# Kernel optimization log

Hardware: AMD Instinct MI355X
Metric: run time of the kernel (lower is better)

The kernel has to match this reference:

```python
import jax, jax.numpy as jnp
import numpy as np

B, L, SH, EH, A, T = 128, 200, 512, 512, 512, 3


def setup_inputs() -> dict:
    key = jax.random.key(0)
    ks = jax.random.split(key, 13)
    s = 0.05  # small init scale to keep tanh/sigmoid unsaturated
    return {
        "sent_enc_doc": jax.random.normal(ks[0], (B, L, 2 * SH), jnp.float32),
        "h0_w": jax.random.normal(ks[1], (EH, SH), jnp.float32) * s,
        "h0_b": jax.random.normal(ks[2], (EH,), jnp.float32) * s,
        "gru_w_ih": jax.random.normal(ks[3], (3 * EH, 2 * SH), jnp.float32) * s,
        "gru_w_hh": jax.random.normal(ks[4], (3 * EH, EH), jnp.float32) * s,
        "gru_b_ih": jax.random.normal(ks[5], (3 * EH,), jnp.float32) * s,
        "gru_b_hh": jax.random.normal(ks[6], (3 * EH,), jnp.float32) * s,
        "wq": jax.random.normal(ks[7], (A, EH), jnp.float32) * s,
        "bq": jax.random.normal(ks[8], (A,), jnp.float32) * s,
        "wd": jax.random.normal(ks[9], (A, 2 * SH), jnp.float32) * s,
        "bd": jax.random.normal(ks[10], (A,), jnp.float32) * s,
        "ws": jax.random.normal(ks[11], (1, A), jnp.float32) * s,
        "bs": jax.random.normal(ks[12], (1,), jnp.float32) * s,
    }


def reference(sent_enc_doc, h0_w, h0_b, gru_w_ih, gru_w_hh, gru_b_ih, gru_b_hh,
              wq, bq, wd, bd, ws, bs):
    b, l, d2 = sent_enc_doc.shape
    sh = d2 // 2
    eh = gru_w_hh.shape[1]
    neg = jnp.asarray(-1e6, sent_enc_doc.dtype)

    # h0 = tanh(W * last backward vector), replicated across doc_len
    last_back = sent_enc_doc[:, 0, sh:]                      # (B, SH)
    h0 = jnp.tanh(last_back @ h0_w.T + h0_b)                 # (B, EH)
    h = jnp.broadcast_to(h0[:, None, :], (b, l, eh))         # (B, L, EH)

    s_prev = jnp.zeros((b, l, d2), sent_enc_doc.dtype)
    d_proj = sent_enc_doc @ wd.T + bd                        # (B, L, A) - loop-invariant
    mask = jnp.zeros((b, l), bool)
    rows = jnp.arange(b)

    scores_list, sel_list = [], []
    for _ in range(T):  # fixed, tiny, sequentially-dependent loop
        # GRUCell (torch gate order: r, z, n)
        gx = s_prev @ gru_w_ih.T + gru_b_ih                  # (B, L, 3EH)
        gh = h @ gru_w_hh.T + gru_b_hh                       # (B, L, 3EH)
        xr, xz, xn = jnp.split(gx, 3, axis=-1)
        hr, hz, hn = jnp.split(gh, 3, axis=-1)
        r = jax.nn.sigmoid(xr + hr)
        z = jax.nn.sigmoid(xz + hz)
        n = jnp.tanh(xn + r * hn)
        h = (1.0 - z) * n + z * h                            # (B, L, EH)

        # scorer: ws . tanh(Wq h + Wd s_i)
        score = (jnp.tanh(h @ wq.T + bq + d_proj) @ ws.T + bs)[..., 0]  # (B, L)
        score = jnp.where(mask, neg, score)
        idx = jnp.argmax(score, axis=1)                      # (B,)
        mask = mask.at[rows, idx].set(True)

        # gather the selected sentence encoding, broadcast to all positions
        s_sel = jnp.take_along_axis(sent_enc_doc, idx[:, None, None], axis=1)  # (B,1,2SH)
        s_prev = jnp.broadcast_to(s_sel, (b, l, d2))

        scores_list.append(score)
        sel_list.append(idx)

    sents_scores = jnp.stack(scores_list, axis=1)            # (B, T, L)
    sents_selected = jnp.stack(sel_list, axis=1)             # (B, T)
    return sents_scores, sents_selected
```

## Files before the change

kernel.cpp:

```cpp
#include <hip/hip_runtime.h>
#include <hip/hip_bf16.h>

constexpr int Bn  = 128;
constexpr int Ln  = 200;
constexpr int D2n = 1024;
constexpr int G3n = 1536;
constexpr int Tn  = 3;
constexpr int Nn  = 512;
constexpr int Kn  = 1024;

typedef unsigned short ushort;
typedef float f32x4 __attribute__((ext_vector_type(4)));
typedef __bf16 bf16x8 __attribute__((ext_vector_type(8)));

__device__ __forceinline__ ushort f2bf(float f) {
  unsigned u = __float_as_uint(f);
  unsigned r = (u + 0x7fffu + ((u >> 16) & 1u)) >> 16;
  return (ushort)r;
}
__device__ __forceinline__ float bf2f(ushort h) {
  return __uint_as_float(((unsigned)h) << 16);
}

__global__ void k_gather_lastb(const float* __restrict__ sent, float* __restrict__ lastb) {
  int i = blockIdx.x * 256 + threadIdx.x;
  int b = i >> 9, k = i & 511;
  lastb[i] = sent[(size_t)b * (Ln * D2n) + 512 + k];
}

__global__ void k_splitW(const float* __restrict__ W, ushort* __restrict__ hi,
                         ushort* __restrict__ lo) {
  int i = blockIdx.x * 256 + threadIdx.x;
  float4 v = ((const float4*)W)[i];
  ushort4 h, l;
  h.x = f2bf(v.x); l.x = f2bf(v.x - bf2f(h.x));
  h.y = f2bf(v.y); l.y = f2bf(v.y - bf2f(h.y));
  h.z = f2bf(v.z); l.z = f2bf(v.z - bf2f(h.z));
  h.w = f2bf(v.w); l.w = f2bf(v.w - bf2f(h.w));
  ((ushort4*)hi)[i] = h;
  ((ushort4*)lo)[i] = l;
}

template<int K, int ACT>
__launch_bounds__(256)
__global__ void k_small_gemm(const float* __restrict__ in, const float* __restrict__ W,
                             const float* __restrict__ bias, float* __restrict__ out, int J) {
  __shared__ float s[16 * K];
  const int b0 = blockIdx.y * 16;
  const int jl = threadIdx.x & 63;
  const int j  = blockIdx.x * 64 + jl;
  const int bg = (threadIdx.x >> 6) * 4;

  const float4* inp4 = (const float4*)(in + (size_t)b0 * K);
  float4* s4 = (float4*)s;
  for (int i = threadIdx.x; i < 4 * K; i += 256) s4[i] = inp4[i];
  __syncthreads();

  const float4* w4 = (const float4*)(W + (size_t)j * K);
  const float4* r0 = (const float4*)(s + (size_t)(bg + 0) * K);
  const float4* r1 = (const float4*)(s + (size_t)(bg + 1) * K);
  const float4* r2 = (const float4*)(s + (size_t)(bg + 2) * K);
  const float4* r3 = (const float4*)(s + (size_t)(bg + 3) * K);

  float acc0 = 0.f, acc1 = 0.f, acc2 = 0.f, acc3 = 0.f;
  #pragma unroll 4
  for (int k4 = 0; k4 < K / 4; ++k4) {
    float4 wv = w4[k4];
    float4 a;
    a = r0[k4]; acc0 += wv.x*a.x + wv.y*a.y + wv.z*a.z + wv.w*a.w;
    a = r1[k4]; acc1 += wv.x*a.x + wv.y*a.y + wv.z*a.z + wv.w*a.w;
    a = r2[k4]; acc2 += wv.x*a.x + wv.y*a.y + wv.z*a.z + wv.w*a.w;
    a = r3[k4]; acc3 += wv.x*a.x + wv.y*a.y + wv.z*a.z + wv.w*a.w;
  }
  float bb = bias[j];
  float v;
  v = acc0 + bb; if (ACT) v = tanhf(v); out[(size_t)(b0 + bg + 0) * J + j] = v;
  v = acc1 + bb; if (ACT) v = tanhf(v); out[(size_t)(b0 + bg + 1) * J + j] = v;
  v = acc2 + bb; if (ACT) v = tanhf(v); out[(size_t)(b0 + bg + 2) * J + j] = v;
  v = acc3 + bb; if (ACT) v = tanhf(v); out[(size_t)(b0 + bg + 3) * J + j] = v;
}

constexpr int LDW = 40;
__launch_bounds__(256)
__global__ void k_dproj_mfma(const float* __restrict__ A, const ushort* __restrict__ Whi,
                             const ushort* __restrict__ Wlo, const float* __restrict__ bias,
                             float* __restrict__ C) {
  __shared__ __align__(16) ushort Ah[128][LDW];
  __shared__ __align__(16) ushort Al[128][LDW];
  __shared__ __align__(16) ushort Bh[128][LDW];
  __shared__ __align__(16) ushort Bl[128][LDW];

  const int m0 = blockIdx.x * 128, n0 = blockIdx.y * 128;
  const int tid  = threadIdx.x;
  const int wave = tid >> 6, lane = tid & 63;
  const int wy = (wave >> 1) * 64, wx = (wave & 1) * 64;
  const int lm = lane & 15, lq = lane >> 4;

  const int sr   = tid >> 1;
  const int sk   = (tid & 1) * 16;

  f32x4 acc[4][4] = {};

  const float* Arow = A + (size_t)(m0 + sr) * Kn + sk;
  const ushort* Bhrow = Whi + (size_t)(n0 + sr) * Kn + sk;
  const ushort* Blrow = Wlo + (size_t)(n0 + sr) * Kn + sk;

  for (int k0 = 0; k0 < Kn; k0 += 32) {
    #pragma unroll
    for (int i = 0; i < 4; ++i) {
      float4 v = *(const float4*)(Arow + k0 + i * 4);
      ushort4 h, l;
      h.x = f2bf(v.x); l.x = f2bf(v.x - bf2f(h.x));
      h.y = f2bf(v.y); l.y = f2bf(v.y - bf2f(h.y));
      h.z = f2bf(v.z); l.z = f2bf(v.z - bf2f(h.z));
      h.w = f2bf(v.w); l.w = f2bf(v.w - bf2f(h.w));
      *(ushort4*)&Ah[sr][sk + i * 4] = h;
      *(ushort4*)&Al[sr][sk + i * 4] = l;
    }
    #pragma unroll
    for (int i = 0; i < 2; ++i) {
      *(int4*)&Bh[sr][sk + i * 8] = *(const int4*)(Bhrow + k0 + i * 8);
      *(int4*)&Bl[sr][sk + i * 8] = *(const int4*)(Blrow + k0 + i * 8);
    }
    __syncthreads();

    bf16x8 ah[4], al[4], bh[4], bl[4];
    #pragma unroll
    for (int mi = 0; mi < 4; ++mi) {
      ah[mi] = *(const bf16x8*)&Ah[wy + mi * 16 + lm][lq * 8];
      al[mi] = *(const bf16x8*)&Al[wy + mi * 16 + lm][lq * 8];
    }
    #pragma unroll
    for (int ni = 0; ni < 4; ++ni) {
      bh[ni] = *(const bf16x8*)&Bh[wx + ni * 16 + lm][lq * 8];
      bl[ni] = *(const bf16x8*)&Bl[wx + ni * 16 + lm][lq * 8];
    }
    #pragma unroll
    for (int mi = 0; mi < 4; ++mi)
      #pragma unroll
      for (int ni = 0; ni < 4; ++ni) {
        acc[mi][ni] = __builtin_amdgcn_mfma_f32_16x16x32_bf16(ah[mi], bh[ni], acc[mi][ni], 0, 0, 0);
        acc[mi][ni] = __builtin_amdgcn_mfma_f32_16x16x32_bf16(ah[mi], bl[ni], acc[mi][ni], 0, 0, 0);
        acc[mi][ni] = __builtin_amdgcn_mfma_f32_16x16x32_bf16(al[mi], bh[ni], acc[mi][ni], 0, 0, 0);
      }
    __syncthreads();
  }

  #pragma unroll
  for (int ni = 0; ni < 4; ++ni) {
    int col = n0 + wx + ni * 16 + lm;
    float bb = bias[col];
    #pragma unroll
    for (int mi = 0; mi < 4; ++mi) {
      int rbase = m0 + wy + mi * 16 + lq * 4;
      #pragma unroll
      for (int r = 0; r < 4; ++r)
        C[(size_t)(rbase + r) * Nn + col] = acc[mi][ni][r] + bb;
    }
  }
}

__global__ void k_gru_pw(const float* __restrict__ gx, const float* __restrict__ gh,
                         float* __restrict__ h) {
  int i = blockIdx.x * 256 + threadIdx.x;
  int b = i >> 9, j = i & 511;
  const float* gxb = gx + (size_t)b * G3n;
  const float* ghb = gh + (size_t)b * G3n;
  float rg = 1.f / (1.f + expf(-(gxb[j] + ghb[j])));
  float zg = 1.f / (1.f + expf(-(gxb[512 + j] + ghb[512 + j])));
  float ng = tanhf(gxb[1024 + j] + rg * ghb[1024 + j]);
  h[i] = (1.f - zg) * ng + zg * h[i];
}

__launch_bounds__(256)
__global__ void k_score(const float* __restrict__ dproj, const float* __restrict__ q,
                        const float* __restrict__ wsv, const float* __restrict__ bsv,
                        const int* __restrict__ mask, float* __restrict__ scoresf,
                        float* __restrict__ outScores, int t) {
  int w = blockIdx.x * 4 + (threadIdx.x >> 6);
  int lane = threadIdx.x & 63;
  int b = w / Ln, l = w % Ln;
  const float4* dp4 = (const float4*)(dproj + (size_t)w * Nn);
  const float4* q4  = (const float4*)(q + (size_t)b * Nn);
  const float4* ws4 = (const float4*)wsv;

  float sum = 0.f;
  #pragma unroll
  for (int i = 0; i < 2; ++i) {
    int idx = lane + i * 64;
    float4 d = dp4[idx], qq = q4[idx], wv = ws4[idx];
    sum += tanhf(qq.x + d.x) * wv.x + tanhf(qq.y + d.y) * wv.y
         + tanhf(qq.z + d.z) * wv.z + tanhf(qq.w + d.w) * wv.w;
  }
  #pragma unroll
  for (int off = 32; off > 0; off >>= 1) sum += __shfl_xor(sum, off, 64);

  if (lane == 0) {
    float v = sum + bsv[0];
    if (mask[w]) v = -1000000.0f;
    scoresf[w] = v;
    outScores[(size_t)b * (Tn * Ln) + t * Ln + l] = v;
  }
}

__launch_bounds__(256)
__global__ void k_argmax(const float* __restrict__ scoresf, const float* __restrict__ sent,
                         float* __restrict__ s_row, int* __restrict__ mask,
                         float* __restrict__ outSel, int t) {
  int b = blockIdx.x;
  __shared__ int s_idx;
  int tid = threadIdx.x;
  if (tid < 64) {
    const float* sc = scoresf + (size_t)b * Ln;
    float best = -3.0e38f; int bi = 0;
    for (int l = tid; l < Ln; l += 64) {
      float v = sc[l];
      if (v > best) { best = v; bi = l; }
    }
    #pragma unroll
    for (int off = 32; off > 0; off >>= 1) {
      float ov = __shfl_down(best, off, 64);
      int   oi = __shfl_down(bi,   off, 64);
      if (ov > best || (ov == best && oi < bi)) { best = ov; bi = oi; }
    }
    if (tid == 0) s_idx = bi;
  }
  __syncthreads();
  int idx = s_idx;
  const float* src = sent + ((size_t)b * Ln + idx) * D2n;
  float* dstp = s_row + (size_t)b * D2n;
  int k = tid * 4;
  *(float4*)(dstp + k) = *(const float4*)(src + k);
  if (tid == 0) {
    mask[b * Ln + idx] = 1;
    outSel[(size_t)b * Tn + t] = (float)idx;
  }
}

extern "C" void kernel_launch(void* const* d_in, const int* in_sizes, int n_in,
                              void* d_out, int out_size, void* d_ws, size_t ws_size,
                              hipStream_t stream) {
  const float* sent = (const float*)d_in[0];
  const float* h0_w = (const float*)d_in[1];
  const float* h0_b = (const float*)d_in[2];
  const float* w_ih = (const float*)d_in[3];
  const float* w_hh = (const float*)d_in[4];
  const float* b_ih = (const float*)d_in[5];
  const float* b_hh = (const float*)d_in[6];
  const float* wq   = (const float*)d_in[7];
  const float* bq   = (const float*)d_in[8];
  const float* wd   = (const float*)d_in[9];
  const float* bd   = (const float*)d_in[10];
  const float* wsv  = (const float*)d_in[11];
  const float* bsv  = (const float*)d_in[12];

  float* wsf     = (float*)d_ws;
  float* d_proj  = wsf;
  float* s_row   = d_proj + 13107200;
  float* h       = s_row + 131072;
  float* gx      = h + 65536;
  float* gh      = gx + 196608;
  float* lastb   = gh + 196608;
  float* q       = lastb + 65536;
  float* scoresf = q + 65536;
  int*   mask    = (int*)(scoresf + 25600);
  ushort* Whi    = (ushort*)(mask + 25600);
  ushort* Wlo    = Whi + 524288;

  float* outScores = (float*)d_out;
  float* outSel    = outScores + (size_t)Bn * Tn * Ln;

  hipMemsetAsync(s_row, 0, 131072 * sizeof(float), stream);
  hipMemsetAsync(mask, 0, 25600 * sizeof(int), stream);

  k_gather_lastb<<<256, 256, 0, stream>>>(sent, lastb);
  k_small_gemm<512, 1><<<dim3(8, 8), 256, 0, stream>>>(lastb, h0_w, h0_b, h, 512);
  k_splitW<<<512, 256, 0, stream>>>(wd, Whi, Wlo);
  k_dproj_mfma<<<dim3(200, 4), 256, 0, stream>>>(sent, Whi, Wlo, bd, d_proj);

  for (int t = 0; t < Tn; ++t) {
    k_small_gemm<1024, 0><<<dim3(24, 8), 256, 0, stream>>>(s_row, w_ih, b_ih, gx, G3n);
    k_small_gemm<512, 0><<<dim3(24, 8), 256, 0, stream>>>(h, w_hh, b_hh, gh, G3n);
    k_gru_pw<<<256, 256, 0, stream>>>(gx, gh, h);
    k_small_gemm<512, 0><<<dim3(8, 8), 256, 0, stream>>>(h, wq, bq, q, 512);
    k_score<<<6400, 256, 0, stream>>>(d_proj, q, wsv, bsv, mask, scoresf, outScores, t);
    k_argmax<<<128, 256, 0, stream>>>(scoresf, sent, s_row, mask, outSel, t);
  }
}
```

Before: 615.0 us.

## Double-buffer d_proj MFMA GEMM with direct global-to-LDS loads and swizzled LDS

Rewrites the loop-invariant d_proj GEMM kernel to double-buffer its LDS tiles. The next k-step's weight tiles stream in through global_load_lds and the fp32 activations are prefetched into registers while the MFMAs run on the current buffer, which drops one barrier per step. LDS rows are unpadded with an XOR swizzle to avoid bank conflicts, and the 2D grid becomes a 1D grid remapped so the tiles running together fall on one N-column of the weights, for L2 reuse. LDS use doubles, which may reduce occupancy, and the swizzle index math has to match exactly between the writers and the fragment readers.

New measurement: 653.5 us. 6.3% more time.

```diff
diff --git a/kernel.cpp b/kernel.cpp
--- a/kernel.cpp
+++ b/kernel.cpp
@@ -12,6 +12,7 @@
 typedef unsigned short ushort;
 typedef float f32x4 __attribute__((ext_vector_type(4)));
 typedef __bf16 bf16x8 __attribute__((ext_vector_type(8)));
+typedef ushort ushort8v __attribute__((ext_vector_type(8)));
 
 __device__ __forceinline__ ushort f2bf(float f) {
   unsigned u = __float_as_uint(f);
@@ -20,6 +21,23 @@
 }
 __device__ __forceinline__ float bf2f(ushort h) {
   return __uint_as_float(((unsigned)h) << 16);
+}
+
+__device__ __forceinline__ void gld_lds16(const ushort* g, ushort* l) {
+  __builtin_amdgcn_global_load_lds(
+      (const __attribute__((address_space(1))) unsigned int*)g,
+      (__attribute__((address_space(3))) unsigned int*)l, 16, 0, 0);
+}
+
+__device__ __forceinline__ void cvt8(const float4 a, const float4 b,
+                                     ushort8v& h, ushort8v& l) {
+  float f[8] = {a.x, a.y, a.z, a.w, b.x, b.y, b.z, b.w};
+  #pragma unroll
+  for (int i = 0; i < 8; ++i) {
+    ushort hi = f2bf(f[i]);
+    h[i] = hi;
+    l[i] = f2bf(f[i] - bf2f(hi));
+  }
 }
 
 __global__ void k_gather_lastb(const float* __restrict__ sent, float* __restrict__ lastb) {
@@ -80,60 +98,90 @@
   v = acc3 + bb; if (ACT) v = tanhf(v); out[(size_t)(b0 + bg + 3) * J + j] = v;
 }
 
-constexpr int LDW = 40;
+constexpr int NSTEP = Kn / 32;
+
 __launch_bounds__(256)
 __global__ void k_dproj_mfma(const float* __restrict__ A, const ushort* __restrict__ Whi,
                              const ushort* __restrict__ Wlo, const float* __restrict__ bias,
                              float* __restrict__ C) {
-  __shared__ __align__(16) ushort Ah[128][LDW];
-  __shared__ __align__(16) ushort Al[128][LDW];
-  __shared__ __align__(16) ushort Bh[128][LDW];
-  __shared__ __align__(16) ushort Bl[128][LDW];
-
-  const int m0 = blockIdx.x * 128, n0 = blockIdx.y * 128;
+  __shared__ __align__(16) ushort sAh[2][128 * 32];
+  __shared__ __align__(16) ushort sAl[2][128 * 32];
+  __shared__ __align__(16) ushort sBh[2][128 * 32];
+  __shared__ __align__(16) ushort sBl[2][128 * 32];
+
+  const int bid = blockIdx.x;
+  const int wg  = (bid & 7) * 100 + (bid >> 3);
+  const int m0  = (wg % 200) * 128;
+  const int n0  = (wg / 200) * 128;
+
   const int tid  = threadIdx.x;
   const int wave = tid >> 6, lane = tid & 63;
   const int wy = (wave >> 1) * 64, wx = (wave & 1) * 64;
   const int lm = lane & 15, lq = lane >> 4;
 
-  const int sr   = tid >> 1;
-  const int sk   = (tid & 1) * 16;
+  const int fs = (lq ^ ((lm >> 1) & 3)) * 8;
+
+  const int sr = tid >> 1;
+  const int sb = (tid & 1) * 2;
+  const int qr = (sr >> 1) & 3;
+  const int ps0 = (sr * 32) + (((sb + 0) ^ qr) * 8);
+  const int ps1 = (sr * 32) + (((sb + 1) ^ qr) * 8);
+  const float* Ap = A + (size_t)(m0 + sr) * Kn + sb * 8;
+
+  const int S0 = (wave * 2 + 0) * 64 + lane;
+  const int S1 = (wave * 2 + 1) * 64 + lane;
+  const int r0 = S0 >> 2, r1 = S1 >> 2;
+  const int c0 = ((S0 & 3) ^ ((r0 >> 1) & 3)) * 8;
+  const int c1 = ((S1 & 3) ^ ((r1 >> 1) & 3)) * 8;
+  const ushort* Bh0 = Whi + (size_t)(n0 + r0) * Kn + c0;
+  const ushort* Bh1 = Whi + (size_t)(n0 + r1) * Kn + c1;
+  const ushort* Bl0 = Wlo + (size_t)(n0 + r0) * Kn + c0;
+  const ushort* Bl1 = Wlo + (size_t)(n0 + r1) * Kn + c1;
+  const int ldsS0 = (wave * 2 + 0) * 512;
+  const int ldsS1 = (wave * 2 + 1) * 512;
 
   f32x4 acc[4][4] = {};
 
-  const float* Arow = A + (size_t)(m0 + sr) * Kn + sk;
-  const ushort* Bhrow = Whi + (size_t)(n0 + sr) * Kn + sk;
-  const ushort* Blrow = Wlo + (size_t)(n0 + sr) * Kn + sk;
-
-  for (int k0 = 0; k0 < Kn; k0 += 32) {
-    #pragma unroll
-    for (int i = 0; i < 4; ++i) {
-      float4 v = *(const float4*)(Arow + k0 + i * 4);
-      ushort4 h, l;
-      h.x = f2bf(v.x); l.x = f2bf(v.x - bf2f(h.x));
-      h.y = f2bf(v.y); l.y = f2bf(v.y - bf2f(h.y));
-      h.z = f2bf(v.z); l.z = f2bf(v.z - bf2f(h.z));
-      h.w = f2bf(v.w); l.w = f2bf(v.w - bf2f(h.w));
-      *(ushort4*)&Ah[sr][sk + i * 4] = h;
-      *(ushort4*)&Al[sr][sk + i * 4] = l;
-    }
-    #pragma unroll
-    for (int i = 0; i < 2; ++i) {
-      *(int4*)&Bh[sr][sk + i * 8] = *(const int4*)(Bhrow + k0 + i * 8);
-      *(int4*)&Bl[sr][sk + i * 8] = *(const int4*)(Blrow + k0 + i * 8);
-    }
+  {
+    gld_lds16(Bh0, &sBh[0][ldsS0]); gld_lds16(Bh1, &sBh[0][ldsS1]);
+    gld_lds16(Bl0, &sBl[0][ldsS0]); gld_lds16(Bl1, &sBl[0][ldsS1]);
+    float4 av[4];
+    #pragma unroll
+    for (int i = 0; i < 4; ++i) av[i] = ((const float4*)Ap)[i];
+    ushort8v h0, l0, h1, l1;
+    cvt8(av[0], av[1], h0, l0);
+    cvt8(av[2], av[3], h1, l1);
+    asm volatile("s_waitcnt vmcnt(0)" ::: "memory");
+    *(ushort8v*)&sAh[0][ps0] = h0;  *(ushort8v*)&sAl[0][ps0] = l0;
+    *(ushort8v*)&sAh[0][ps1] = h1;  *(ushort8v*)&sAl[0][ps1] = l1;
+  }
+
+  for (int ks = 0; ks < NSTEP; ++ks) {
+    const int cur = ks & 1, nxt = cur ^ 1;
     __syncthreads();
 
+    const int kn = (ks + 1) * 32;
+    const bool pf = (ks + 1 < NSTEP);
+    float4 av[4];
+    if (pf) {
+      gld_lds16(Bh0 + kn, &sBh[nxt][ldsS0]); gld_lds16(Bh1 + kn, &sBh[nxt][ldsS1]);
+      gld_lds16(Bl0 + kn, &sBl[nxt][ldsS0]); gld_lds16(Bl1 + kn, &sBl[nxt][ldsS1]);
+      #pragma unroll
+      for (int i = 0; i < 4; ++i) av[i] = ((const float4*)(Ap + kn))[i];
+    }
+
     bf16x8 ah[4], al[4], bh[4], bl[4];
     #pragma unroll
     for (int mi = 0; mi < 4; ++mi) {
-      ah[mi] = *(const bf16x8*)&Ah[wy + mi * 16 + lm][lq * 8];
-      al[mi] = *(const bf16x8*)&Al[wy + mi * 16 + lm][lq * 8];
+      const int o = (wy + mi * 16 + lm) * 32 + fs;
+      ah[mi] = *(const bf16x8*)&sAh[cur][o];
+      al[mi] = *(const bf16x8*)&sAl[cur][o];
     }
     #pragma unroll
     for (int ni = 0; ni < 4; ++ni) {
-      bh[ni] = *(const bf16x8*)&Bh[wx + ni * 16 + lm][lq * 8];
-      bl[ni] = *(const bf16x8*)&Bl[wx + ni * 16 + lm][lq * 8];
+      const int o = (wx + ni * 16 + lm) * 32 + fs;
+      bh[ni] = *(const bf16x8*)&sBh[cur][o];
+      bl[ni] = *(const bf16x8*)&sBl[cur][o];
     }
     #pragma unroll
     for (int mi = 0; mi < 4; ++mi)
@@ -143,7 +191,15 @@
         acc[mi][ni] = __builtin_amdgcn_mfma_f32_16x16x32_bf16(ah[mi], bl[ni], acc[mi][ni], 0, 0, 0);
         acc[mi][ni] = __builtin_amdgcn_mfma_f32_16x16x32_bf16(al[mi], bh[ni], acc[mi][ni], 0, 0, 0);
       }
-    __syncthreads();
+
+    if (pf) {
+      ushort8v h0, l0, h1, l1;
+      cvt8(av[0], av[1], h0, l0);
+      cvt8(av[2], av[3], h1, l1);
+      asm volatile("s_waitcnt vmcnt(0)" ::: "memory");
+      *(ushort8v*)&sAh[nxt][ps0] = h0;  *(ushort8v*)&sAl[nxt][ps0] = l0;
+      *(ushort8v*)&sAh[nxt][ps1] = h1;  *(ushort8v*)&sAl[nxt][ps1] = l1;
+    }
   }
 
   #pragma unroll
@@ -276,7 +332,7 @@
   k_gather_lastb<<<256, 256, 0, stream>>>(sent, lastb);
   k_small_gemm<512, 1><<<dim3(8, 8), 256, 0, stream>>>(lastb, h0_w, h0_b, h, 512);
   k_splitW<<<512, 256, 0, stream>>>(wd, Whi, Wlo);
-  k_dproj_mfma<<<dim3(200, 4), 256, 0, stream>>>(sent, Whi, Wlo, bd, d_proj);
+  k_dproj_mfma<<<800, 256, 0, stream>>>(sent, Whi, Wlo, bd, d_proj);
 
   for (int t = 0; t < Tn; ++t) {
     k_small_gemm<1024, 0><<<dim3(24, 8), 256, 0, stream>>>(s_row, w_ih, b_ih, gx, G3n);
```

## Pre-split activations to bf16 hi/lo and stream tiles via global_load_lds with XOR swizzle

Applied to the files above, without the earlier changes.

Adds a separate pass that splits the full sent_enc_doc activation into bf16 hi/lo arrays, so the d_proj MFMA GEMM no longer converts fp32 to bf16 inside its main loop. Tiles are then loaded straight from global memory into LDS with global_load_lds, using an XOR-swizzled, unpadded LDS layout to avoid bank conflicts. The grid is flattened to 1D with M-fastest block ordering. The cost is an extra 100MB of bf16 intermediates to write and read back, in place of reading 100MB of fp32 once.

New measurement: 619.3 us. No clear change (+0.7%).

```diff
diff --git a/kernel.cpp b/kernel.cpp
--- a/kernel.cpp
+++ b/kernel.cpp
@@ -22,14 +22,20 @@
   return __uint_as_float(((unsigned)h) << 16);
 }
 
+__device__ __forceinline__ void gld_lds16(const ushort* g, ushort* l) {
+  __builtin_amdgcn_global_load_lds(
+      (const __attribute__((address_space(1))) unsigned int*)g,
+      (__attribute__((address_space(3))) unsigned int*)l, 16, 0, 0);
+}
+
 __global__ void k_gather_lastb(const float* __restrict__ sent, float* __restrict__ lastb) {
   int i = blockIdx.x * 256 + threadIdx.x;
   int b = i >> 9, k = i & 511;
   lastb[i] = sent[(size_t)b * (Ln * D2n) + 512 + k];
 }
 
-__global__ void k_splitW(const float* __restrict__ W, ushort* __restrict__ hi,
-                         ushort* __restrict__ lo) {
+__global__ void k_split(const float* __restrict__ W, ushort* __restrict__ hi,
+                        ushort* __restrict__ lo) {
   int i = blockIdx.x * 256 + threadIdx.x;
   float4 v = ((const float4*)W)[i];
   ushort4 h, l;
@@ -80,60 +86,68 @@
   v = acc3 + bb; if (ACT) v = tanhf(v); out[(size_t)(b0 + bg + 3) * J + j] = v;
 }
 
-constexpr int LDW = 40;
+constexpr int NSTEP = Kn / 32;
+
 __launch_bounds__(256)
-__global__ void k_dproj_mfma(const float* __restrict__ A, const ushort* __restrict__ Whi,
-                             const ushort* __restrict__ Wlo, const float* __restrict__ bias,
-                             float* __restrict__ C) {
-  __shared__ __align__(16) ushort Ah[128][LDW];
-  __shared__ __align__(16) ushort Al[128][LDW];
-  __shared__ __align__(16) ushort Bh[128][LDW];
-  __shared__ __align__(16) ushort Bl[128][LDW];
-
-  const int m0 = blockIdx.x * 128, n0 = blockIdx.y * 128;
+__global__ void k_dproj_mfma(const ushort* __restrict__ Ahi, const ushort* __restrict__ Alo,
+                             const ushort* __restrict__ Whi, const ushort* __restrict__ Wlo,
+                             const float* __restrict__ bias, float* __restrict__ C) {
+  __shared__ __align__(16) ushort sAh[128 * 32];
+  __shared__ __align__(16) ushort sAl[128 * 32];
+  __shared__ __align__(16) ushort sBh[128 * 32];
+  __shared__ __align__(16) ushort sBl[128 * 32];
+
+  const int bid = blockIdx.x;
+  const int m0  = (bid % 200) * 128;
+  const int n0  = (bid / 200) * 128;
+
   const int tid  = threadIdx.x;
   const int wave = tid >> 6, lane = tid & 63;
   const int wy = (wave >> 1) * 64, wx = (wave & 1) * 64;
   const int lm = lane & 15, lq = lane >> 4;
 
-  const int sr   = tid >> 1;
-  const int sk   = (tid & 1) * 16;
+  const int fs = (lq ^ ((lm >> 1) & 3)) * 8;
+
+  const int S0 = (wave * 2 + 0) * 64 + lane;
+  const int S1 = (wave * 2 + 1) * 64 + lane;
+  const int r0 = S0 >> 2, r1 = S1 >> 2;
+  const int c0 = ((S0 & 3) ^ ((r0 >> 1) & 3)) * 8;
+  const int c1 = ((S1 & 3) ^ ((r1 >> 1) & 3)) * 8;
+  const ushort* pAh0 = Ahi + (size_t)(m0 + r0) * Kn + c0;
+  const ushort* pAh1 = Ahi + (size_t)(m0 + r1) * Kn + c1;
+  const ushort* pAl0 = Alo + (size_t)(m0 + r0) * Kn + c0;
+  const ushort* pAl1 = Alo + (size_t)(m0 + r1) * Kn + c1;
+  const ushort* pBh0 = Whi + (size_t)(n0 + r0) * Kn + c0;
+  const ushort* pBh1 = Whi + (size_t)(n0 + r1) * Kn + c1;
+  const ushort* pBl0 = Wlo + (size_t)(n0 + r0) * Kn + c0;
+  const ushort* pBl1 = Wlo + (size_t)(n0 + r1) * Kn + c1;
+  ushort* dA0 = &sAh[S0 * 8]; ushort* dA1 = &sAh[S1 * 8];
+  ushort* dL0 = &sAl[S0 * 8]; ushort* dL1 = &sAl[S1 * 8];
+  ushort* dB0 = &sBh[S0 * 8]; ushort* dB1 = &sBh[S1 * 8];
+  ushort* dC0 = &sBl[S0 * 8]; ushort* dC1 = &sBl[S1 * 8];
 
   f32x4 acc[4][4] = {};
 
-  const float* Arow = A + (size_t)(m0 + sr) * Kn + sk;
-  const ushort* Bhrow = Whi + (size_t)(n0 + sr) * Kn + sk;
-  const ushort* Blrow = Wlo + (size_t)(n0 + sr) * Kn + sk;
-
-  for (int k0 = 0; k0 < Kn; k0 += 32) {
-    #pragma unroll
-    for (int i = 0; i < 4; ++i) {
-      float4 v = *(const float4*)(Arow + k0 + i * 4);
-      ushort4 h, l;
-      h.x = f2bf(v.x); l.x = f2bf(v.x - bf2f(h.x));
-      h.y = f2bf(v.y); l.y = f2bf(v.y - bf2f(h.y));
-      h.z = f2bf(v.z); l.z = f2bf(v.z - bf2f(h.z));
-      h.w = f2bf(v.w); l.w = f2bf(v.w - bf2f(h.w));
-      *(ushort4*)&Ah[sr][sk + i * 4] = h;
-      *(ushort4*)&Al[sr][sk + i * 4] = l;
-    }
-    #pragma unroll
-    for (int i = 0; i < 2; ++i) {
-      *(int4*)&Bh[sr][sk + i * 8] = *(const int4*)(Bhrow + k0 + i * 8);
-      *(int4*)&Bl[sr][sk + i * 8] = *(const int4*)(Blrow + k0 + i * 8);
-    }
+  for (int ks = 0; ks < NSTEP; ++ks) {
+    const int ko = ks * 32;
+    gld_lds16(pAh0 + ko, dA0); gld_lds16(pAh1 + ko, dA1);
+    gld_lds16(pAl0 + ko, dL0); gld_lds16(pAl1 + ko, dL1);
+    gld_lds16(pBh0 + ko, dB0); gld_lds16(pBh1 + ko, dB1);
+    gld_lds16(pBl0 + ko, dC0); gld_lds16(pBl1 + ko, dC1);
     __syncthreads();
 
     bf16x8 ah[4], al[4], bh[4], bl[4];
     #pragma unroll
     for (int mi = 0; mi < 4; ++mi) {
-      ah[mi] = *(const bf16x8*)&Ah[wy + mi * 16 + lm][lq * 8];
-      al[mi] = *(const bf16x8*)&Al[wy + mi * 16 + lm][lq * 8];
+      const int o = (wy + mi * 16 + lm) * 32 + fs;
+      ah[mi] = *(const bf16x8*)&sAh[o];
+      al[mi] = *(const bf16x8*)&sAl[o];
     }
     #pragma unroll
     for (int ni = 0; ni < 4; ++ni) {
-      bh[ni] = *(const bf16x8*)&Bh[wx + ni * 16 + lm][lq * 8];
-      bl[ni] = *(const bf16x8*)&Bl[wx + ni * 16 + lm][lq * 8];
+      const int o = (wx + ni * 16 + lm) * 32 + fs;
+      bh[ni] = *(const bf16x8*)&sBh[o];
+      bl[ni] = *(const bf16x8*)&sBl[o];
     }
     #pragma unroll
     for (int mi = 0; mi < 4; ++mi)
@@ -266,6 +280,8 @@
   int*   mask    = (int*)(scoresf + 25600);
   ushort* Whi    = (ushort*)(mask + 25600);
   ushort* Wlo    = Whi + 524288;
+  ushort* Ahi    = Wlo + 524288;
+  ushort* Alo    = Ahi + 26214400;
 
   float* outScores = (float*)d_out;
   float* outSel    = outScores + (size_t)Bn * Tn * Ln;
@@ -275,8 +291,9 @@
 
   k_gather_lastb<<<256, 256, 0, stream>>>(sent, lastb);
   k_small_gemm<512, 1><<<dim3(8, 8), 256, 0, stream>>>(lastb, h0_w, h0_b, h, 512);
-  k_splitW<<<512, 256, 0, stream>>>(wd, Whi, Wlo);
-  k_dproj_mfma<<<dim3(200, 4), 256, 0, stream>>>(sent, Whi, Wlo, bd, d_proj);
+  k_split<<<512, 256, 0, stream>>>(wd, Whi, Wlo);
+  k_split<<<25600, 256, 0, stream>>>(sent, Ahi, Alo);
+  k_dproj_mfma<<<800, 256, 0, stream>>>(Ahi, Alo, Whi, Wlo, bd, d_proj);
 
   for (int t = 0; t < Tn; ++t) {
     k_small_gemm<1024, 0><<<dim3(24, 8), 256, 0, stream>>>(s_row, w_ih, b_ih, gx, G3n);
```
